# Kernel tuning notes

Measured on AMD Instinct MI355X. Metric: run time of the kernel, lower is better.

The kernel has to match this reference:

```python
import jax, jax.numpy as jnp
import numpy as np

N_NODES = 100000
N_EDGES = 600000
N_GRAPHS = 512
X_DIM = 2
E_DIM = 2
U_DIM = 2


def setup_inputs() -> dict:
    key = jax.random.key(0)
    ks = jax.random.split(key, 16)
    inp = {
        "x": jax.random.normal(ks[0], (N_NODES, X_DIM), jnp.float32),
        "edge_index": jax.random.randint(ks[1], (2, N_EDGES), 0, N_NODES, jnp.int64),
        "edge_attr": jax.random.normal(ks[2], (N_EDGES, E_DIM), jnp.float32),
        "u": jax.random.normal(ks[3], (N_GRAPHS, U_DIM), jnp.float32),
        "batch": jnp.sort(jax.random.randint(ks[4], (N_NODES,), 0, N_GRAPHS, jnp.int64)),
    }
    def lin(k, fin, fout):
        bound = 1.0 / np.sqrt(fin)
        kw, kb = jax.random.split(k)
        W = jax.random.uniform(kw, (fin, fout), jnp.float32, -bound, bound)
        b = jax.random.uniform(kb, (fout,), jnp.float32, -bound, bound)
        return W, b
    inp["W1a"], inp["b1a"] = lin(ks[5], X_DIM + E_DIM, 64)
    inp["W1b"], inp["b1b"] = lin(ks[6], 64, 128)
    inp["W2a"], inp["b2a"] = lin(ks[7], X_DIM + 128 + U_DIM, 256)
    inp["W2b"], inp["b2b"] = lin(ks[8], 256, 512)
    return inp


def reference(x, edge_index, edge_attr, u, batch, W1a, b1a, W1b, b1b, W2a, b2a, W2b, b2b):
    row, col = edge_index[0], edge_index[1]
    n = x.shape[0]
    # gather + concat -> MLP1 over edges: [E, 4] -> [E, 128]
    e_in = jnp.concatenate([x[col], edge_attr], axis=1)
    h = jnp.maximum(e_in @ W1a + b1a, 0.0) @ W1b + b1b
    # scatter_mean over destination nodes (row)
    s = jax.ops.segment_sum(h, row, num_segments=n)
    cnt = jax.ops.segment_sum(jnp.ones((row.shape[0], 1), h.dtype), row, num_segments=n)
    agg = s / jnp.maximum(cnt, 1.0)
    # node-level concat -> MLP2: [N, 132] -> [N, 512]
    z = jnp.concatenate([x, agg, u[batch]], axis=1)
    return jnp.maximum(z @ W2a + b2a, 0.0) @ W2b + b2b
```

## Files before the change

kernel.cpp:

```cpp
#include <hip/hip_runtime.h>

#define NN 100000
#define NE 600000
#define NP 100096
#define NB 391
#define NBE 9375

typedef float v4    __attribute__((ext_vector_type(4)));
typedef float f32x4 __attribute__((ext_vector_type(4)));
typedef short s16x4 __attribute__((ext_vector_type(4)));
typedef short s16x8 __attribute__((ext_vector_type(8)));

__device__ __forceinline__ short f2bf(float f) {
    unsigned u = __float_as_uint(f);
    u = (u + 0x7fffu + ((u >> 16) & 1u)) >> 16;
    return (short)u;
}
__device__ __forceinline__ float bf2f(unsigned short v) {
    return __uint_as_float(((unsigned)v) << 16);
}

__global__ __launch_bounds__(256) void hist_prep_kernel(
    const int* __restrict__ ei, int* __restrict__ deg,
    const float* __restrict__ W2a, const float* __restrict__ W2b,
    const float* __restrict__ W1a, const float* __restrict__ W1b,
    short* __restrict__ W2aF, short* __restrict__ W2bF,
    short* __restrict__ W1aT, short* __restrict__ W1bT)
{
    int idx = blockIdx.x * 256 + threadIdx.x;
    if (idx < NE) atomicAdd(&deg[ei[idx]], 1);

    if (idx < 16 * 5 * 512) {
        int j = idx & 7;
        int lane = (idx >> 3) & 63;
        int t2 = idx >> 9;
        int ks = t2 % 5, nb = t2 / 5;
        int n = nb * 16 + (lane & 15);
        int k = ks * 32 + (lane >> 4) * 8 + j;
        float v = 0.f;
        if (k < 128)       v = W2a[(2 + k) * 256 + n];
        else if (k == 128) v = W2a[0 * 256 + n];
        else if (k == 129) v = W2a[1 * 256 + n];
        else if (k == 130) v = W2a[130 * 256 + n];
        else if (k == 131) v = W2a[131 * 256 + n];
        W2aF[idx] = f2bf(v);
    }
    if (idx < 32 * 8 * 512) {
        int j = idx & 7;
        int lane = (idx >> 3) & 63;
        int t2 = idx >> 9;
        int ks = t2 & 7, nb = t2 >> 3;
        int n = nb * 16 + (lane & 15);
        int k = ks * 32 + (lane >> 4) * 8 + j;
        W2bF[idx] = f2bf(W2b[k * 512 + n]);
    }
    if (idx < 64 * 32) {
        int n = idx >> 5, k = idx & 31;
        W1aT[idx] = (k < 4) ? f2bf(W1a[k * 64 + n]) : (short)0;
    }
    if (idx < 128 * 64) {
        int n = idx >> 6, k = idx & 63;
        W1bT[idx] = f2bf(W1b[k * 128 + n]);
    }
}

__global__ __launch_bounds__(256) void scan1_kernel(const int* __restrict__ deg,
                                                    int* __restrict__ partial,
                                                    int* __restrict__ bsum) {
    __shared__ int tmp[256];
    int t = threadIdx.x;
    int i = blockIdx.x * 256 + t;
    int v = deg[i];
    tmp[t] = v;
    __syncthreads();
    for (int off = 1; off < 256; off <<= 1) {
        int add = (t >= off) ? tmp[t - off] : 0;
        __syncthreads();
        tmp[t] += add;
        __syncthreads();
    }
    partial[i] = tmp[t] - v;
    if (t == 255) bsum[blockIdx.x] = tmp[255];
}

__global__ __launch_bounds__(512) void scan2_kernel(const int* __restrict__ bsum,
                                                    int* __restrict__ boff) {
    __shared__ int tmp[512];
    int t = threadIdx.x;
    int v = (t < NB) ? bsum[t] : 0;
    tmp[t] = v;
    __syncthreads();
    for (int off = 1; off < 512; off <<= 1) {
        int add = (t >= off) ? tmp[t - off] : 0;
        __syncthreads();
        tmp[t] += add;
        __syncthreads();
    }
    boff[t] = tmp[t] - v;
}

__global__ __launch_bounds__(256) void fill_kernel(const int* __restrict__ ei,
                                                   const float* __restrict__ x,
                                                   const float* __restrict__ ea,
                                                   const int* __restrict__ partial,
                                                   const int* __restrict__ boff,
                                                   int* __restrict__ cnt2,
                                                   int* __restrict__ rowp,
                                                   short* __restrict__ in_csr) {
    int e = blockIdx.x * 256 + threadIdx.x;
    if (e < NE) {
        int r = ei[e];
        int c = ei[NE + e];
        int p = partial[r] + boff[r >> 8] + atomicAdd(&cnt2[r], 1);
        rowp[p] = r;
        s16x8 v = {0, 0, 0, 0, 0, 0, 0, 0};
        v[0] = f2bf(x[2 * c]);  v[1] = f2bf(x[2 * c + 1]);
        v[2] = f2bf(ea[2 * e]); v[3] = f2bf(ea[2 * e + 1]);
        *(s16x8*)&in_csr[(size_t)p * 8] = v;
    }
}

__global__ __launch_bounds__(256, 8) void edge_fused_kernel(
    const short* __restrict__ in_csr, const int* __restrict__ rowp,
    const short* __restrict__ W1aT, const short* __restrict__ W1bT,
    const float* __restrict__ b1a, const float* __restrict__ b1b,
    const int* __restrict__ partial, const int* __restrict__ boff,
    const int* __restrict__ deg,
    short* __restrict__ aggb, float* __restrict__ pstart,
    float* __restrict__ pend)
{
    __shared__ short pool[64 * 136];
    __shared__ int   rows[64];
    __shared__ float midlo[128], midhi[128];
    short* t1  = pool;
    short* hbf = pool;
    const int tid = threadIdx.x;
    const int p0 = blockIdx.x * 64;

    if (tid < 64) rows[tid] = rowp[p0 + tid];

    const int lane = tid & 63, nw = tid >> 6;
    const int l15 = lane & 15, lk = lane >> 4;

    f32x4 a1[4];
#pragma unroll
    for (int bf = 0; bf < 4; ++bf) a1[bf] = (f32x4){0.f, 0.f, 0.f, 0.f};
    {
        s16x8 wA = *(const s16x8*)&W1aT[(nw * 16 + l15) * 32 + lk * 8];
        s16x8 zz = {0, 0, 0, 0, 0, 0, 0, 0};
#pragma unroll
        for (int bf = 0; bf < 4; ++bf) {
            s16x8 bI = zz;
            if (lk == 0)
                bI = *(const s16x8*)&in_csr[(size_t)(p0 + bf * 16 + l15) * 8];
            a1[bf] = __builtin_amdgcn_mfma_f32_16x16x32_bf16(wA, bI, a1[bf], 0, 0, 0);
        }
    }
    {
        f32x4 bias = *(const f32x4*)&b1a[nw * 16 + lk * 4];
#pragma unroll
        for (int bf = 0; bf < 4; ++bf) {
            s16x4 pk;
#pragma unroll
            for (int j = 0; j < 4; ++j)
                pk[j] = f2bf(fmaxf(a1[bf][j] + bias[j], 0.f));
            *(s16x4*)&t1[(bf * 16 + l15) * 72 + nw * 16 + lk * 4] = pk;
        }
    }
    __syncthreads();

    f32x4 a2[2][4];
#pragma unroll
    for (int af = 0; af < 2; ++af)
#pragma unroll
        for (int bf = 0; bf < 4; ++bf) a2[af][bf] = (f32x4){0.f, 0.f, 0.f, 0.f};

#pragma unroll
    for (int ks = 0; ks < 2; ++ks) {
        s16x8 w[2], b[4];
#pragma unroll
        for (int af = 0; af < 2; ++af)
            w[af] = *(const s16x8*)&W1bT[((nw * 2 + af) * 16 + l15) * 64 + ks * 32 + lk * 8];
#pragma unroll
        for (int bf = 0; bf < 4; ++bf)
            b[bf] = *(const s16x8*)&t1[(bf * 16 + l15) * 72 + ks * 32 + lk * 8];
#pragma unroll
        for (int af = 0; af < 2; ++af)
#pragma unroll
            for (int bf = 0; bf < 4; ++bf)
                a2[af][bf] = __builtin_amdgcn_mfma_f32_16x16x32_bf16(
                    w[af], b[bf], a2[af][bf], 0, 0, 0);
    }
    __syncthreads();

#pragma unroll
    for (int af = 0; af < 2; ++af) {
        int oc0 = (nw * 2 + af) * 16 + lk * 4;
        f32x4 bias = *(const f32x4*)&b1b[oc0];
#pragma unroll
        for (int bf = 0; bf < 4; ++bf) {
            s16x4 pk;
#pragma unroll
            for (int j = 0; j < 4; ++j)
                pk[j] = f2bf(a2[af][bf][j] + bias[j]);
            *(s16x4*)&hbf[(bf * 16 + l15) * 136 + oc0] = pk;
        }
    }
    __syncthreads();

    {
        const int half = tid >> 7;
        const int c = tid & 127;
        const int slo = half * 32, shi = slo + 32;
        float sum = 0.f;
        int cur = rows[slo];
        bool first = true;
        for (int i = slo; i < shi; ++i) {
            sum += bf2f((unsigned short)hbf[i * 136 + c]);
            bool segend = (i == shi - 1) || (rows[i + 1] != cur);
            if (segend) {
                bool crossMid  = (half == 0) && (i == 31) && (rows[32] == cur);
                bool fromLower = (half == 1) && first && (rows[31] == cur);
                if (crossMid) {
                    midlo[c] = sum;
                } else if (fromLower) {
                    midhi[c] = sum;
                } else {
                    int bs = partial[cur] + boff[cur >> 8];
                    int d = deg[cur];
                    bool sh = bs >= p0, eh = bs + d <= p0 + 64;
                    if (sh && eh)      aggb[(size_t)cur * 128 + c] = f2bf(sum / (float)d);
                    else if (sh)       pend[(size_t)blockIdx.x * 128 + c] = sum;
                    else if (eh)       pstart[(size_t)blockIdx.x * 128 + c] = sum;
                }
                sum = 0.f;
                first = false;
                if (i < shi - 1) cur = rows[i + 1];
            }
        }
    }
    __syncthreads();
    if (tid < 128 && rows[31] == rows[32]) {
        int c = tid, cur = rows[32];
        float s = midlo[c] + midhi[c];
        int bs = partial[cur] + boff[cur >> 8];
        int d = deg[cur];
        bool sh = bs >= p0, eh = bs + d <= p0 + 64;
        if (sh && eh)      aggb[(size_t)cur * 128 + c] = f2bf(s / (float)d);
        else if (sh)       pend[(size_t)blockIdx.x * 128 + c] = s;
        else if (eh)       pstart[(size_t)blockIdx.x * 128 + c] = s;
    }
}

__global__ __launch_bounds__(512, 4) void node_mfma_kernel(
    const float* __restrict__ x, const float* __restrict__ u,
    const int* __restrict__ batch,
    const short* __restrict__ aggb,
    const int* __restrict__ deg, const int* __restrict__ partial,
    const int* __restrict__ boff,
    const float* __restrict__ pstart, const float* __restrict__ pend,
    const short* __restrict__ W2aF, const short* __restrict__ W2bF,
    const float* __restrict__ b2a, const float* __restrict__ b2b,
    float* __restrict__ out)
{
    __shared__ short lds[64 * 256];
    __shared__ int   rmode[64];
    __shared__ float rinv[64];
    __shared__ int   rk[64];
    const int tid = threadIdx.x;
    const int node0 = blockIdx.x * 64;

    if (tid < 64) {
        int node = node0 + tid;
        int mode = 0, k = 0;
        float inv = 0.f;
        if (node < NN) {
            int d = deg[node];
            if (d > 0) {
                int bs = partial[node] + boff[node >> 8];
                k = bs >> 6;
                mode = ((bs & 63) + d > 64) ? 2 : 1;
                inv = 1.0f / (float)d;
            }
        }
        rmode[tid] = mode; rinv[tid] = inv; rk[tid] = k;
    }
    __syncthreads();

#pragma unroll
    for (int it = 0; it < 2; ++it) {
        int idx = it * 512 + tid;
        int r = idx >> 4, ch = idx & 15;
        int node = node0 + r;
        int mode = rmode[r];
        s16x8 v = {0, 0, 0, 0, 0, 0, 0, 0};
        if (mode == 1) {
            v = *(const s16x8*)&aggb[(size_t)node * 128 + ch * 8];
        } else if (mode == 2) {
            float inv = rinv[r];
            int k = rk[r];
            const float* pe = &pend[(size_t)k * 128 + ch * 8];
            const float* ps = &pstart[(size_t)(k + 1) * 128 + ch * 8];
#pragma unroll
            for (int j = 0; j < 8; ++j)
                v[j] = f2bf((pe[j] + ps[j]) * inv);
        }
        int sw = (ch & ~7) | ((ch ^ r) & 7);
        *(s16x8*)&lds[r * 192 + sw * 8] = v;
    }
    if (tid < 64) {
        int r = tid, node = node0 + r;
        s16x8 p = {0, 0, 0, 0, 0, 0, 0, 0};
        if (node < NN) {
            p[0] = f2bf(x[node * 2]); p[1] = f2bf(x[node * 2 + 1]);
            int b = batch[node];
            p[2] = f2bf(u[b * 2]); p[3] = f2bf(u[b * 2 + 1]);
        }
        int sw = 16 | (r & 7);
        *(s16x8*)&lds[r * 192 + sw * 8] = p;
    } else if (tid < 256) {
        int t2 = tid - 64;
        int r = t2 & 63;
        int ch = 17 + (t2 >> 6);
        int sw = (ch & ~7) | ((ch ^ r) & 7);
        s16x8 zz = {0, 0, 0, 0, 0, 0, 0, 0};
        *(s16x8*)&lds[r * 192 + sw * 8] = zz;
    }
    __syncthreads();

    const int lane = tid & 63, nw = tid >> 6;
    const int l15 = lane & 15, lk = lane >> 4;

    f32x4 acc1[4][2];
#pragma unroll
    for (int mf = 0; mf < 4; ++mf)
#pragma unroll
        for (int nf = 0; nf < 2; ++nf)
            acc1[mf][nf] = (f32x4){0.f, 0.f, 0.f, 0.f};

#pragma unroll
    for (int ks = 0; ks < 5; ++ks) {
        s16x8 a[4], w[2];
        int cb = ks * 4 + lk;
#pragma unroll
        for (int mf = 0; mf < 4; ++mf) {
            int r = mf * 16 + l15;
            int sw = (cb & ~7) | ((cb ^ r) & 7);
            a[mf] = *(const s16x8*)&lds[r * 192 + sw * 8];
        }
#pragma unroll
        for (int nf = 0; nf < 2; ++nf)
            w[nf] = *(const s16x8*)&W2aF[((((nw * 2 + nf) * 5) + ks) * 64 + lane) * 8];
#pragma unroll
        for (int mf = 0; mf < 4; ++mf)
#pragma unroll
            for (int nf = 0; nf < 2; ++nf)
                acc1[mf][nf] = __builtin_amdgcn_mfma_f32_16x16x32_bf16(
                    w[nf], a[mf], acc1[mf][nf], 0, 0, 0);
    }
    __syncthreads();

#pragma unroll
    for (int nf = 0; nf < 2; ++nf) {
        int n0 = nw * 32 + nf * 16 + lk * 4;
        f32x4 bias = *(const f32x4*)&b2a[n0];
        int ch = n0 >> 3, off = n0 & 7;
#pragma unroll
        for (int mf = 0; mf < 4; ++mf) {
            int m = mf * 16 + l15;
            s16x4 pk;
#pragma unroll
            for (int j = 0; j < 4; ++j)
                pk[j] = f2bf(fmaxf(acc1[mf][nf][j] + bias[j], 0.f));
            int sw = (ch & ~7) | ((ch ^ m) & 7);
            *(s16x4*)&lds[m * 256 + sw * 8 + off] = pk;
        }
    }
    __syncthreads();

    f32x4 acc2[4][4];
#pragma unroll
    for (int mf = 0; mf < 4; ++mf)
#pragma unroll
        for (int nf = 0; nf < 4; ++nf)
            acc2[mf][nf] = (f32x4){0.f, 0.f, 0.f, 0.f};

#pragma unroll
    for (int ks = 0; ks < 8; ++ks) {
        s16x8 b[4], w[4];
        int cb = ks * 4 + lk;
#pragma unroll
        for (int mf = 0; mf < 4; ++mf) {
            int r = mf * 16 + l15;
            int sw = (cb & ~7) | ((cb ^ r) & 7);
            b[mf] = *(const s16x8*)&lds[r * 256 + sw * 8];
        }
#pragma unroll
        for (int nf = 0; nf < 4; ++nf)
            w[nf] = *(const s16x8*)&W2bF[((((nw * 4 + nf) * 8) + ks) * 64 + lane) * 8];
#pragma unroll
        for (int mf = 0; mf < 4; ++mf)
#pragma unroll
            for (int nf = 0; nf < 4; ++nf)
                acc2[mf][nf] = __builtin_amdgcn_mfma_f32_16x16x32_bf16(
                    w[nf], b[mf], acc2[mf][nf], 0, 0, 0);
    }

#pragma unroll
    for (int nf = 0; nf < 4; ++nf) {
        int n0 = nw * 64 + nf * 16 + lk * 4;
        f32x4 bias = *(const f32x4*)&b2b[n0];
#pragma unroll
        for (int mf = 0; mf < 4; ++mf) {
            int node = node0 + mf * 16 + l15;
            if (node < NN) {
                f32x4 o = acc2[mf][nf] + bias;
                __builtin_nontemporal_store(o, (f32x4*)&out[(size_t)node * 512 + n0]);
            }
        }
    }
}

extern "C" void kernel_launch(void* const* d_in, const int* in_sizes, int n_in,
                              void* d_out, int out_size, void* d_ws, size_t ws_size,
                              hipStream_t stream) {
    const float* x          = (const float*)d_in[0];
    const int*   edge_index = (const int*)d_in[1];
    const float* edge_attr  = (const float*)d_in[2];
    const float* u          = (const float*)d_in[3];
    const int*   batch      = (const int*)d_in[4];
    const float* W1a        = (const float*)d_in[5];
    const float* b1a        = (const float*)d_in[6];
    const float* W1b        = (const float*)d_in[7];
    const float* b1b        = (const float*)d_in[8];
    const float* W2a        = (const float*)d_in[9];
    const float* b2a        = (const float*)d_in[10];
    const float* W2b        = (const float*)d_in[11];
    const float* b2b        = (const float*)d_in[12];
    float* out = (float*)d_out;

    short* aggb   = (short*)d_ws;
    short* W2aF   = aggb + (size_t)NN * 128;
    short* W2bF   = W2aF + 16 * 5 * 512;
    short* W1aT   = W2bF + 32 * 8 * 512;
    short* W1bT   = W1aT + 64 * 32;
    int*   deg    = (int*)(W1bT + 128 * 64);
    int*   cnt2   = deg + NP;
    int*   partial= cnt2 + NP;
    int*   bsum   = partial + NP;
    int*   boff   = bsum + 512;
    int*   rowp   = boff + 512;
    float* pstart = (float*)(rowp + NE);
    float* pend   = pstart + (size_t)NBE * 128;
    short* in_csr = (short*)(pend + (size_t)NBE * 128);

    hipMemsetAsync(deg, 0, 2 * NP * sizeof(int), stream);

    hist_prep_kernel<<<(NE + 255) / 256, 256, 0, stream>>>(
        edge_index, deg, W2a, W2b, W1a, W1b, W2aF, W2bF, W1aT, W1bT);
    scan1_kernel<<<NB, 256, 0, stream>>>(deg, partial, bsum);
    scan2_kernel<<<1, 512, 0, stream>>>(bsum, boff);
    fill_kernel <<<(NE + 255) / 256, 256, 0, stream>>>(edge_index, x, edge_attr,
                                                       partial, boff, cnt2,
                                                       rowp, in_csr);

    edge_fused_kernel<<<NBE, 256, 0, stream>>>(
        in_csr, rowp, W1aT, W1bT, b1a, b1b,
        partial, boff, deg, aggb, pstart, pend);

    node_mfma_kernel<<<(NN + 63) / 64, 512, 0, stream>>>(
        x, u, batch, aggb, deg, partial, boff, pstart, pend,
        W2aF, W2bF, b2a, b2b, out);
}
```

Baseline: 211.1 us.

## Move aggregate fixup and x/u packing out of node MFMA kernel; load A from global

Precomputes packed bf16 [x, u[batch]] rows in the histogram kernel and adds a separate fixup kernel that resolves split-segment partial sums (and zero-degree rows) into aggb in place. The node MLP kernel then reads A fragments directly from global aggb/xu instead of staging them through LDS, removing a preamble, two syncs and per-row mode logic. The cost is an extra kernel launch and an extra pass over aggb. The direct global fragment loads are less coalesced than the previous staged copy.

```diff
diff --git a/kernel.cpp b/kernel.cpp
--- a/kernel.cpp
+++ b/kernel.cpp
@@ -22,13 +22,24 @@
 
 __global__ __launch_bounds__(256) void hist_prep_kernel(
     const int* __restrict__ ei, int* __restrict__ deg,
+    const float* __restrict__ x, const float* __restrict__ u,
+    const int* __restrict__ batch,
     const float* __restrict__ W2a, const float* __restrict__ W2b,
     const float* __restrict__ W1a, const float* __restrict__ W1b,
     short* __restrict__ W2aF, short* __restrict__ W2bF,
-    short* __restrict__ W1aT, short* __restrict__ W1bT)
+    short* __restrict__ W1aT, short* __restrict__ W1bT,
+    short* __restrict__ xu)
 {
     int idx = blockIdx.x * 256 + threadIdx.x;
     if (idx < NE) atomicAdd(&deg[ei[idx]], 1);
+
+    if (idx < NN) {
+        s16x8 p = {0, 0, 0, 0, 0, 0, 0, 0};
+        p[0] = f2bf(x[2 * idx]); p[1] = f2bf(x[2 * idx + 1]);
+        int b = batch[idx];
+        p[2] = f2bf(u[2 * b]); p[3] = f2bf(u[2 * b + 1]);
+        *(s16x8*)&xu[(size_t)idx * 8] = p;
+    }
 
     if (idx < 16 * 5 * 512) {
         int j = idx & 7;
@@ -252,82 +263,44 @@
     }
 }
 
-__global__ __launch_bounds__(512, 4) void node_mfma_kernel(
-    const float* __restrict__ x, const float* __restrict__ u,
-    const int* __restrict__ batch,
-    const short* __restrict__ aggb,
+__global__ __launch_bounds__(256) void fixup_kernel(
     const int* __restrict__ deg, const int* __restrict__ partial,
     const int* __restrict__ boff,
     const float* __restrict__ pstart, const float* __restrict__ pend,
+    short* __restrict__ aggb)
+{
+    int idx = blockIdx.x * 256 + threadIdx.x;
+    int n = idx >> 4, ch = idx & 15;
+    if (n >= NN) return;
+    int d = deg[n];
+    if (d == 0) {
+        s16x8 z = {0, 0, 0, 0, 0, 0, 0, 0};
+        *(s16x8*)&aggb[(size_t)n * 128 + ch * 8] = z;
+        return;
+    }
+    int bs = partial[n] + boff[n >> 8];
+    if ((bs & 63) + d > 64) {
+        int k = bs >> 6;
+        float inv = 1.0f / (float)d;
+        const float* pe = &pend[(size_t)k * 128 + ch * 8];
+        const float* ps = &pstart[(size_t)(k + 1) * 128 + ch * 8];
+        s16x8 v;
+#pragma unroll
+        for (int j = 0; j < 8; ++j)
+            v[j] = f2bf((pe[j] + ps[j]) * inv);
+        *(s16x8*)&aggb[(size_t)n * 128 + ch * 8] = v;
+    }
+}
+
+__global__ __launch_bounds__(512, 4) void node_mfma_kernel(
+    const short* __restrict__ aggb, const short* __restrict__ xu,
     const short* __restrict__ W2aF, const short* __restrict__ W2bF,
     const float* __restrict__ b2a, const float* __restrict__ b2b,
     float* __restrict__ out)
 {
-    __shared__ short lds[64 * 256];
-    __shared__ int   rmode[64];
-    __shared__ float rinv[64];
-    __shared__ int   rk[64];
+    __shared__ short tb[64 * 256];
     const int tid = threadIdx.x;
     const int node0 = blockIdx.x * 64;
-
-    if (tid < 64) {
-        int node = node0 + tid;
-        int mode = 0, k = 0;
-        float inv = 0.f;
-        if (node < NN) {
-            int d = deg[node];
-            if (d > 0) {
-                int bs = partial[node] + boff[node >> 8];
-                k = bs >> 6;
-                mode = ((bs & 63) + d > 64) ? 2 : 1;
-                inv = 1.0f / (float)d;
-            }
-        }
-        rmode[tid] = mode; rinv[tid] = inv; rk[tid] = k;
-    }
-    __syncthreads();
-
-#pragma unroll
-    for (int it = 0; it < 2; ++it) {
-        int idx = it * 512 + tid;
-        int r = idx >> 4, ch = idx & 15;
-        int node = node0 + r;
-        int mode = rmode[r];
-        s16x8 v = {0, 0, 0, 0, 0, 0, 0, 0};
-        if (mode == 1) {
-            v = *(const s16x8*)&aggb[(size_t)node * 128 + ch * 8];
-        } else if (mode == 2) {
-            float inv = rinv[r];
-            int k = rk[r];
-            const float* pe = &pend[(size_t)k * 128 + ch * 8];
-            const float* ps = &pstart[(size_t)(k + 1) * 128 + ch * 8];
-#pragma unroll
-            for (int j = 0; j < 8; ++j)
-                v[j] = f2bf((pe[j] + ps[j]) * inv);
-        }
-        int sw = (ch & ~7) | ((ch ^ r) & 7);
-        *(s16x8*)&lds[r * 192 + sw * 8] = v;
-    }
-    if (tid < 64) {
-        int r = tid, node = node0 + r;
-        s16x8 p = {0, 0, 0, 0, 0, 0, 0, 0};
-        if (node < NN) {
-            p[0] = f2bf(x[node * 2]); p[1] = f2bf(x[node * 2 + 1]);
-            int b = batch[node];
-            p[2] = f2bf(u[b * 2]); p[3] = f2bf(u[b * 2 + 1]);
-        }
-        int sw = 16 | (r & 7);
-        *(s16x8*)&lds[r * 192 + sw * 8] = p;
-    } else if (tid < 256) {
-        int t2 = tid - 64;
-        int r = t2 & 63;
-        int ch = 17 + (t2 >> 6);
-        int sw = (ch & ~7) | ((ch ^ r) & 7);
-        s16x8 zz = {0, 0, 0, 0, 0, 0, 0, 0};
-        *(s16x8*)&lds[r * 192 + sw * 8] = zz;
-    }
-    __syncthreads();
-
     const int lane = tid & 63, nw = tid >> 6;
     const int l15 = lane & 15, lk = lane >> 4;
 
@@ -341,12 +314,17 @@
 #pragma unroll
     for (int ks = 0; ks < 5; ++ks) {
         s16x8 a[4], w[2];
-        int cb = ks * 4 + lk;
 #pragma unroll
         for (int mf = 0; mf < 4; ++mf) {
-            int r = mf * 16 + l15;
-            int sw = (cb & ~7) | ((cb ^ r) & 7);
-            a[mf] = *(const s16x8*)&lds[r * 192 + sw * 8];
+            int node = node0 + mf * 16 + l15;
+            if (ks < 4) {
+                a[mf] = *(const s16x8*)&aggb[(size_t)node * 128 + ks * 32 + lk * 8];
+            } else {
+                s16x8 z = {0, 0, 0, 0, 0, 0, 0, 0};
+                a[mf] = z;
+                if (lk == 0)
+                    a[mf] = *(const s16x8*)&xu[(size_t)node * 8];
+            }
         }
 #pragma unroll
         for (int nf = 0; nf < 2; ++nf)
@@ -358,7 +336,6 @@
                 acc1[mf][nf] = __builtin_amdgcn_mfma_f32_16x16x32_bf16(
                     w[nf], a[mf], acc1[mf][nf], 0, 0, 0);
     }
-    __syncthreads();
 
 #pragma unroll
     for (int nf = 0; nf < 2; ++nf) {
@@ -373,7 +350,7 @@
             for (int j = 0; j < 4; ++j)
                 pk[j] = f2bf(fmaxf(acc1[mf][nf][j] + bias[j], 0.f));
             int sw = (ch & ~7) | ((ch ^ m) & 7);
-            *(s16x4*)&lds[m * 256 + sw * 8 + off] = pk;
+            *(s16x4*)&tb[m * 256 + sw * 8 + off] = pk;
         }
     }
     __syncthreads();
@@ -393,7 +370,7 @@
         for (int mf = 0; mf < 4; ++mf) {
             int r = mf * 16 + l15;
             int sw = (cb & ~7) | ((cb ^ r) & 7);
-            b[mf] = *(const s16x8*)&lds[r * 256 + sw * 8];
+            b[mf] = *(const s16x8*)&tb[r * 256 + sw * 8];
         }
 #pragma unroll
         for (int nf = 0; nf < 4; ++nf)
@@ -440,7 +417,8 @@
     float* out = (float*)d_out;
 
     short* aggb   = (short*)d_ws;
-    short* W2aF   = aggb + (size_t)NN * 128;
+    short* xu     = aggb + (size_t)NP * 128;
+    short* W2aF   = xu + (size_t)NP * 8;
     short* W2bF   = W2aF + 16 * 5 * 512;
     short* W1aT   = W2bF + 32 * 8 * 512;
     short* W1bT   = W1aT + 64 * 32;
@@ -457,7 +435,8 @@
     hipMemsetAsync(deg, 0, 2 * NP * sizeof(int), stream);
 
     hist_prep_kernel<<<(NE + 255) / 256, 256, 0, stream>>>(
-        edge_index, deg, W2a, W2b, W1a, W1b, W2aF, W2bF, W1aT, W1bT);
+        edge_index, deg, x, u, batch, W2a, W2b, W1a, W1b,
+        W2aF, W2bF, W1aT, W1bT, xu);
     scan1_kernel<<<NB, 256, 0, stream>>>(deg, partial, bsum);
     scan2_kernel<<<1, 512, 0, stream>>>(bsum, boff);
     fill_kernel <<<(NE + 255) / 256, 256, 0, stream>>>(edge_index, x, edge_attr,
@@ -468,7 +447,9 @@
         in_csr, rowp, W1aT, W1bT, b1a, b1b,
         partial, boff, deg, aggb, pstart, pend);
 
+    fixup_kernel<<<(NN * 16 + 255) / 256, 256, 0, stream>>>(
+        deg, partial, boff, pstart, pend, aggb);
+
     node_mfma_kernel<<<(NN + 63) / 64, 512, 0, stream>>>(
-        x, u, batch, aggb, deg, partial, boff, pstart, pend,
-        W2aF, W2bF, b2a, b2b, out);
-}
+        aggb, xu, W2aF, W2bF, b2a, b2b, out);
+}
```

New measurement: 230.3 us. +9.1%, slower.
